# Kernel tuning notes

Hardware: AMD Instinct MI355X
Metric: run time of the kernel (lower is better)

## Reference

```python
import jax, jax.numpy as jnp
import numpy as np

C = 256
POOL = 4

def setup_inputs() -> dict:
    key = jax.random.key(0)
    ks = jax.random.split(key, 8)
    B, H, W = 4, 256, 256
    d = C // 8
    x = jax.random.normal(ks[0], (B, C, H, W), dtype=jnp.float32)
    # 1x1 conv weights stored as [out, in] matrices (kernel_size=1)
    s = 1.0 / np.sqrt(C)
    Wq = jax.random.uniform(ks[1], (d, C), jnp.float32, -s, s)
    bq = jax.random.uniform(ks[2], (d,), jnp.float32, -s, s)
    Wk = jax.random.uniform(ks[3], (d, C), jnp.float32, -s, s)
    bk = jax.random.uniform(ks[4], (d,), jnp.float32, -s, s)
    Wv = jax.random.uniform(ks[5], (C, C), jnp.float32, -s, s)
    bv = jax.random.uniform(ks[6], (C,), jnp.float32, -s, s)
    gamma = jax.random.normal(ks[7], (1,), jnp.float32) * 0.1
    return {"x": x, "Wq": Wq, "bq": bq, "Wk": Wk, "bk": bk,
            "Wv": Wv, "bv": bv, "gamma": gamma}


def reference(x, Wq, bq, Wk, bk, Wv, bv, gamma):
    B, Cc, H, W = x.shape
    Hp, Wp = H // POOL, W // POOL
    # AvgPool2d(kernel=4, stride=4)
    xp = x.reshape(B, Cc, Hp, POOL, Wp, POOL).mean(axis=(3, 5))  # [B,C,Hp,Wp]
    xf = xp.reshape(B, Cc, Hp * Wp)                              # [B,C,N]
    # 1x1 convs == channel matmuls
    q = jnp.einsum('dc,bcn->bdn', Wq, xf) + bq[None, :, None]    # [B,d,N]
    k = jnp.einsum('dc,bcn->bdn', Wk, xf) + bk[None, :, None]    # [B,d,N]
    v = jnp.einsum('ec,bcn->ben', Wv, xf) + bv[None, :, None]    # [B,C,N]
    # energy[b,n,m] = q[:, :, n] . k[:, :, m]
    energy = jnp.einsum('bdn,bdm->bnm', q, k)                    # [B,N,N]
    attn = jax.nn.softmax(energy, axis=-1)
    # out = v @ attn^T  -> out[b,c,n] = sum_m v[b,c,m] * attn[b,n,m]
    out = jnp.einsum('bcm,bnm->bcn', v, attn)                    # [B,C,N]
    out = out.reshape(B, Cc, Hp, Wp)
    # bilinear upsample, half-pixel centers (align_corners=False)
    up = jax.image.resize(out, (B, Cc, H, W), method='bilinear')
    return gamma[0] * up + x
```

## Files before the change

### kernel.cpp

```cpp
#include <hip/hip_runtime.h>

#define B_ 4
#define C_ 256
#define N_ 4096
#define D_ 32

typedef __bf16 bf16;
typedef __bf16 bf16x4 __attribute__((ext_vector_type(4)));
typedef __bf16 bf16x8 __attribute__((ext_vector_type(8)));
typedef float f32x4 __attribute__((ext_vector_type(4)));

__global__ __launch_bounds__(256) void k_prep(
    const float* __restrict__ Wq, const float* __restrict__ bq,
    const float* __restrict__ Wk, const float* __restrict__ bk,
    const float* __restrict__ Wv, const float* __restrict__ bv,
    bf16* __restrict__ wt, float* __restrict__ bias) {
  int r = blockIdx.x, t = threadIdx.x;
  const float* src; float bval;
  if (r < 32)      { src = Wq + (r << 8);        bval = bq[r]; }
  else if (r < 64) { src = Wk + ((r - 32) << 8); bval = bk[r - 32]; }
  else             { src = Wv + ((r - 64) << 8); bval = bv[r - 64]; }
  wt[(r << 8) + t] = (bf16)src[t];
  if (t == 0) bias[r] = bval;
}

__global__ __launch_bounds__(1024) void k_fused(const float* __restrict__ x,
    const bf16* __restrict__ wt, const float* __restrict__ bias,
    bf16* __restrict__ qt, bf16* __restrict__ kt, bf16* __restrict__ v) {
  __shared__ bf16 xsb[64][264];
  int tid = threadIdx.x, wave = tid >> 6, l = tid & 63;
  int lg = l >> 4, ll = l & 15;
  int b = blockIdx.x >> 6, hp = blockIdx.x & 63, n0 = hp * 64;

  const float4* x4 = reinterpret_cast<const float4*>(x) +
      ((size_t)((b * 256 + wave * 16) * 256 + hp * 4)) * 64 + l;
  for (int c0 = 0; c0 < 16; c0 += 4) {
    float s[4] = {0.f, 0.f, 0.f, 0.f};
    #pragma unroll
    for (int j = 0; j < 4; ++j) {
      const float4* p = x4 + (size_t)(c0 + j) * 16384;
      #pragma unroll
      for (int dh = 0; dh < 4; ++dh) {
        float4 a = p[dh * 64];
        s[j] += a.x + a.y + a.z + a.w;
      }
    }
    bf16x4 pk;
    #pragma unroll
    for (int j = 0; j < 4; ++j) pk[j] = (bf16)(s[j] * 0.0625f);
    *reinterpret_cast<bf16x4*>(&xsb[l][wave * 16 + c0]) = pk;
  }
  __syncthreads();

  f32x4 acc[2][4];
  #pragma unroll
  for (int j = 0; j < 2; ++j)
    #pragma unroll
    for (int cb = 0; cb < 4; ++cb) acc[j][cb] = (f32x4){0.f, 0.f, 0.f, 0.f};

  for (int kk = 0; kk < 8; ++kk) {
    bf16x8 bfr[4];
    #pragma unroll
    for (int cb = 0; cb < 4; ++cb)
      bfr[cb] = *reinterpret_cast<const bf16x8*>(&xsb[cb * 16 + ll][kk * 32 + lg * 8]);
    #pragma unroll
    for (int j = 0; j < 2; ++j) {
      int rb = wave + j * 16;
      if (rb < 20) {
        bf16x8 afr = *reinterpret_cast<const bf16x8*>(
            wt + ((size_t)(rb * 16 + ll)) * 256 + kk * 32 + lg * 8);
        #pragma unroll
        for (int cb = 0; cb < 4; ++cb)
          acc[j][cb] = __builtin_amdgcn_mfma_f32_16x16x32_bf16(afr, bfr[cb], acc[j][cb], 0, 0, 0);
      }
    }
  }

  #pragma unroll
  for (int j = 0; j < 2; ++j) {
    int rb = wave + j * 16;
    if (rb < 20) {
      int row0 = rb * 16 + lg * 4;
      float4 b4 = *reinterpret_cast<const float4*>(bias + row0);
      #pragma unroll
      for (int cb = 0; cb < 4; ++cb) {
        int n = n0 + cb * 16 + ll;
        float v0 = acc[j][cb][0] + b4.x, v1 = acc[j][cb][1] + b4.y;
        float v2 = acc[j][cb][2] + b4.z, v3 = acc[j][cb][3] + b4.w;
        if (row0 < 32) {
          bf16x4 pk = {(bf16)v0, (bf16)v1, (bf16)v2, (bf16)v3};
          *reinterpret_cast<bf16x4*>(qt + ((size_t)(b * N_ + n)) * D_ + row0) = pk;
        } else if (row0 < 64) {
          bf16x4 pk = {(bf16)v0, (bf16)v1, (bf16)v2, (bf16)v3};
          *reinterpret_cast<bf16x4*>(kt + ((size_t)(b * N_ + n)) * D_ + row0 - 32) = pk;
        } else {
          int c = row0 - 64;
          v[((size_t)(b * 256 + c + 0)) * N_ + n] = (bf16)v0;
          v[((size_t)(b * 256 + c + 1)) * N_ + n] = (bf16)v1;
          v[((size_t)(b * 256 + c + 2)) * N_ + n] = (bf16)v2;
          v[((size_t)(b * 256 + c + 3)) * N_ + n] = (bf16)v3;
        }
      }
    }
  }
}

__global__ __launch_bounds__(1024) void k_attn(const bf16* __restrict__ qt,
    const bf16* __restrict__ kt, const bf16* __restrict__ v,
    float* __restrict__ outs) {
  __shared__ bf16 p_s[64][264];
  __shared__ float l_red[16][64];
  __shared__ float l_s[64];
  int tid = threadIdx.x, wave = tid >> 6, l = tid & 63;
  int lg = l >> 4, ll = l & 15;
  int blk = blockIdx.x;
  int b  = (blk & 7) >> 1;
  int nt = ((blk >> 3) << 1) | (blk & 1);
  int n0 = nt * 64;

  const f32x4 fz = {0.f, 0.f, 0.f, 0.f};

  bf16x8 aq[4];
  #pragma unroll
  for (int tnf = 0; tnf < 4; ++tnf)
    aq[tnf] = *reinterpret_cast<const bf16x8*>(
        qt + ((size_t)(b * N_ + n0 + tnf * 16 + ll)) * D_ + lg * 8);

  f32x4 acc[4];
  float lsum[4][4];
  #pragma unroll
  for (int a = 0; a < 4; ++a) {
    acc[a] = fz;
    #pragma unroll
    for (int r = 0; r < 4; ++r) lsum[a][r] = 0.f;
  }

  const int mw = wave * 16;
  for (int t = 0; t < 16; ++t) {
    int m0 = t * 256;
    {
      int mglob = m0 + mw + ll;
      bf16x8 bk8 = *reinterpret_cast<const bf16x8*>(
          kt + ((size_t)(b * N_ + mglob)) * D_ + lg * 8);
      #pragma unroll
      for (int tnf = 0; tnf < 4; ++tnf) {
        f32x4 e = __builtin_amdgcn_mfma_f32_16x16x32_bf16(aq[tnf], bk8, fz, 0, 0, 0);
        int col = mw + ll;
        #pragma unroll
        for (int r = 0; r < 4; ++r) {
          float p = __expf(e[r]);
          lsum[tnf][r] += p;
          p_s[tnf * 16 + lg * 4 + r][col] = (bf16)p;
        }
      }
    }
    __syncthreads();
    #pragma unroll
    for (int kk = 0; kk < 8; ++kk) {
      bf16x8 bv8 = *reinterpret_cast<const bf16x8*>(
          v + ((size_t)((b << 8) + mw + ll)) * N_ + m0 + kk * 32 + lg * 8);
      #pragma unroll
      for (int tnf = 0; tnf < 4; ++tnf) {
        bf16x8 pa = *reinterpret_cast<const bf16x8*>(
            &p_s[tnf * 16 + ll][kk * 32 + lg * 8]);
        acc[tnf] = __builtin_amdgcn_mfma_f32_16x16x32_bf16(pa, bv8, acc[tnf], 0, 0, 0);
      }
    }
    __syncthreads();
  }

  #pragma unroll
  for (int tnf = 0; tnf < 4; ++tnf) {
    #pragma unroll
    for (int r = 0; r < 4; ++r) {
      float s = lsum[tnf][r];
      s += __shfl_xor(s, 1);
      s += __shfl_xor(s, 2);
      s += __shfl_xor(s, 4);
      s += __shfl_xor(s, 8);
      if (ll == 0) l_red[wave][tnf * 16 + lg * 4 + r] = s;
    }
  }
  __syncthreads();
  if (tid < 64) {
    float s = 0.f;
    #pragma unroll
    for (int w = 0; w < 16; ++w) s += l_red[w][tid];
    l_s[tid] = s;
  }
  __syncthreads();

  int c = mw + ll;
  #pragma unroll
  for (int tnf = 0; tnf < 4; ++tnf) {
    int tn0 = tnf * 16 + lg * 4;
    float4 o;
    o.x = acc[tnf][0] / l_s[tn0 + 0];
    o.y = acc[tnf][1] / l_s[tn0 + 1];
    o.z = acc[tnf][2] / l_s[tn0 + 2];
    o.w = acc[tnf][3] / l_s[tn0 + 3];
    *reinterpret_cast<float4*>(outs + ((size_t)((b << 8) + c)) * N_ + n0 + tn0) = o;
  }
}

__global__ __launch_bounds__(256) void k_up(const float* __restrict__ outs,
    const float* __restrict__ x, const float* __restrict__ gamma,
    float* __restrict__ out) {
  __shared__ float s_o[4096];
  int tid = threadIdx.x, wave = tid >> 6, tw = tid & 63;
  int bc = blockIdx.x;
  const float* src = outs + (size_t)bc * 4096;
  #pragma unroll
  for (int ch = 0; ch < 4; ++ch)
    *reinterpret_cast<float4*>(&s_o[ch * 1024 + tid * 4]) =
        *reinterpret_cast<const float4*>(src + ch * 1024 + tid * 4);
  __syncthreads();

  float g = gamma[0];
  const float4* xr = reinterpret_cast<const float4*>(x) + (size_t)bc * 16384;
  float4* outr = reinterpret_cast<float4*>(out) + (size_t)bc * 16384;

  int twm = tw == 0 ? 0 : tw - 1;
  int twp = tw == 63 ? 63 : tw + 1;

  for (int hb = 0; hb < 64; ++hb) {
    int h = hb * 4 + wave;
    int th = 2 * h - 3;
    int h0 = th < 0 ? -1 : (th >> 3);
    float fh = (float)(th - 8 * h0) * 0.125f;
    int i0h = h0 < 0 ? 0 : h0;
    int i1h = h0 + 1 > 63 ? 63 : h0 + 1;
    const float* r0 = &s_o[i0h * 64];
    const float* r1 = &s_o[i1h * 64];
    float a_m = r0[twm], a_c = r0[tw], a_p = r0[twp];
    float b_m = r1[twm], b_c = r1[tw], b_p = r1[twp];
    float t0 = a_m + 0.625f * (a_c - a_m), u0 = b_m + 0.625f * (b_c - b_m);
    float t1 = a_m + 0.875f * (a_c - a_m), u1 = b_m + 0.875f * (b_c - b_m);
    float t2 = a_c + 0.125f * (a_p - a_c), u2 = b_c + 0.125f * (b_p - b_c);
    float t3 = a_c + 0.375f * (a_p - a_c), u3 = b_c + 0.375f * (b_p - b_c);
    float4 xv = xr[h * 64 + tw];
    float4 o;
    o.x = g * (t0 + fh * (u0 - t0)) + xv.x;
    o.y = g * (t1 + fh * (u1 - t1)) + xv.y;
    o.z = g * (t2 + fh * (u2 - t2)) + xv.z;
    o.w = g * (t3 + fh * (u3 - t3)) + xv.w;
    outr[h * 64 + tw] = o;
  }
}

extern "C" void kernel_launch(void* const* d_in, const int* in_sizes, int n_in,
                              void* d_out, int out_size, void* d_ws, size_t ws_size,
                              hipStream_t stream) {
  const float* x     = (const float*)d_in[0];
  const float* Wq    = (const float*)d_in[1];
  const float* bq    = (const float*)d_in[2];
  const float* Wk    = (const float*)d_in[3];
  const float* bk    = (const float*)d_in[4];
  const float* Wv    = (const float*)d_in[5];
  const float* bv    = (const float*)d_in[6];
  const float* gamma = (const float*)d_in[7];
  float* out = (float*)d_out;

  char* ws = (char*)d_ws;
  float* outs = (float*)(ws);
  bf16*  v    = (bf16*) (ws + (16u << 20));
  bf16*  qt   = (bf16*) (ws + (24u << 20));
  bf16*  kt   = (bf16*) (ws + (25u << 20));
  bf16*  wt   = (bf16*) (ws + (26u << 20));
  float* bias = (float*)(ws + (27u << 20));

  hipLaunchKernelGGL(k_prep,  dim3(320),  dim3(256),  0, stream,
                     Wq, bq, Wk, bk, Wv, bv, wt, bias);
  hipLaunchKernelGGL(k_fused, dim3(256),  dim3(1024), 0, stream,
                     x, wt, bias, qt, kt, v);
  hipLaunchKernelGGL(k_attn,  dim3(256),  dim3(1024), 0, stream, qt, kt, v, outs);
  hipLaunchKernelGGL(k_up,    dim3(1024), dim3(256),  0, stream, outs, x, gamma, out);
}
```

Before: 259.6 us.

## Double-buffer attention probabilities to overlap QK exp with PV MFMA

```diff
diff --git a/kernel.cpp b/kernel.cpp
--- a/kernel.cpp
+++ b/kernel.cpp
@@ -108,7 +108,7 @@
 __global__ __launch_bounds__(1024) void k_attn(const bf16* __restrict__ qt,
     const bf16* __restrict__ kt, const bf16* __restrict__ v,
     float* __restrict__ outs) {
-  __shared__ bf16 p_s[64][264];
+  __shared__ bf16 p_s[2][64][264];
   __shared__ float l_red[16][64];
   __shared__ float l_s[64];
   int tid = threadIdx.x, wave = tid >> 6, l = tid & 63;
@@ -136,37 +136,65 @@
   }
 
   const int mw = wave * 16;
-  for (int t = 0; t < 16; ++t) {
+  const int colw = mw + ll;
+
+  {
+    bf16x8 bk8 = *reinterpret_cast<const bf16x8*>(
+        kt + ((size_t)(b * N_ + colw)) * D_ + lg * 8);
+    #pragma unroll
+    for (int tnf = 0; tnf < 4; ++tnf) {
+      f32x4 e = __builtin_amdgcn_mfma_f32_16x16x32_bf16(aq[tnf], bk8, fz, 0, 0, 0);
+      #pragma unroll
+      for (int r = 0; r < 4; ++r) {
+        float p = __expf(e[r]);
+        lsum[tnf][r] += p;
+        p_s[0][tnf * 16 + lg * 4 + r][colw] = (bf16)p;
+      }
+    }
+  }
+  __syncthreads();
+
+  for (int t = 0; t < 15; ++t) {
     int m0 = t * 256;
-    {
-      int mglob = m0 + mw + ll;
-      bf16x8 bk8 = *reinterpret_cast<const bf16x8*>(
-          kt + ((size_t)(b * N_ + mglob)) * D_ + lg * 8);
-      #pragma unroll
-      for (int tnf = 0; tnf < 4; ++tnf) {
-        f32x4 e = __builtin_amdgcn_mfma_f32_16x16x32_bf16(aq[tnf], bk8, fz, 0, 0, 0);
-        int col = mw + ll;
-        #pragma unroll
-        for (int r = 0; r < 4; ++r) {
-          float p = __expf(e[r]);
-          lsum[tnf][r] += p;
-          p_s[tnf * 16 + lg * 4 + r][col] = (bf16)p;
-        }
-      }
-    }
-    __syncthreads();
+    int cur = t & 1, nxt = cur ^ 1;
+    bf16x8 bk8 = *reinterpret_cast<const bf16x8*>(
+        kt + ((size_t)(b * N_ + m0 + 256 + colw)) * D_ + lg * 8);
     #pragma unroll
     for (int kk = 0; kk < 8; ++kk) {
       bf16x8 bv8 = *reinterpret_cast<const bf16x8*>(
-          v + ((size_t)((b << 8) + mw + ll)) * N_ + m0 + kk * 32 + lg * 8);
+          v + ((size_t)((b << 8) + colw)) * N_ + m0 + kk * 32 + lg * 8);
       #pragma unroll
       for (int tnf = 0; tnf < 4; ++tnf) {
         bf16x8 pa = *reinterpret_cast<const bf16x8*>(
-            &p_s[tnf * 16 + ll][kk * 32 + lg * 8]);
+            &p_s[cur][tnf * 16 + ll][kk * 32 + lg * 8]);
         acc[tnf] = __builtin_amdgcn_mfma_f32_16x16x32_bf16(pa, bv8, acc[tnf], 0, 0, 0);
       }
     }
+    #pragma unroll
+    for (int tnf = 0; tnf < 4; ++tnf) {
+      f32x4 e = __builtin_amdgcn_mfma_f32_16x16x32_bf16(aq[tnf], bk8, fz, 0, 0, 0);
+      #pragma unroll
+      for (int r = 0; r < 4; ++r) {
+        float p = __expf(e[r]);
+        lsum[tnf][r] += p;
+        p_s[nxt][tnf * 16 + lg * 4 + r][colw] = (bf16)p;
+      }
+    }
     __syncthreads();
+  }
+  {
+    int m0 = 15 * 256;
+    #pragma unroll
+    for (int kk = 0; kk < 8; ++kk) {
+      bf16x8 bv8 = *reinterpret_cast<const bf16x8*>(
+          v + ((size_t)((b << 8) + colw)) * N_ + m0 + kk * 32 + lg * 8);
+      #pragma unroll
+      for (int tnf = 0; tnf < 4; ++tnf) {
+        bf16x8 pa = *reinterpret_cast<const bf16x8*>(
+            &p_s[1][tnf * 16 + ll][kk * 32 + lg * 8]);
+        acc[tnf] = __builtin_amdgcn_mfma_f32_16x16x32_bf16(pa, bv8, acc[tnf], 0, 0, 0);
+      }
+    }
   }
 
   #pragma unroll
@@ -190,7 +218,6 @@
   }
   __syncthreads();
 
-  int c = mw + ll;
   #pragma unroll
   for (int tnf = 0; tnf < 4; ++tnf) {
     int tn0 = tnf * 16 + lg * 4;
@@ -199,7 +226,7 @@
     o.y = acc[tnf][1] / l_s[tn0 + 1];
     o.z = acc[tnf][2] / l_s[tn0 + 2];
     o.w = acc[tnf][3] / l_s[tn0 + 3];
-    *reinterpret_cast<float4*>(outs + ((size_t)((b << 8) + c)) * N_ + n0 + tn0) = o;
+    *reinterpret_cast<float4*>(outs + ((size_t)((b << 8) + colw)) * N_ + n0 + tn0) = o;
   }
 }
 
```

Result: faster. 253.1 us (-2.5%).
